# Optimization experiments

Measured on AMD Instinct MI355X. Metric: run time of the kernel, lower is better.

Reference implementation:

```python
import jax, jax.numpy as jnp
import numpy as np

NUM_CLASSES = 3
EPS = 1e-6
POS_IOU = 0.5   # assumed thresholds of utils.match_anchors_to_targets
NEG_IOU = 0.4
NEG_RATIO = 3


def _make_anchors(H, W, stride):
    sizes = np.array([3.0, 4.0, 5.0]) * stride  # 3 anchors per location
    ys = (np.arange(H) + 0.5) * stride
    xs = (np.arange(W) + 0.5) * stride
    cy, cx = np.meshgrid(ys, xs, indexing='ij')
    cx = cx[:, :, None]
    cy = cy[:, :, None]
    s = sizes[None, None, :]
    boxes = np.stack([cx - s / 2, cy - s / 2, cx + s / 2, cy + s / 2], axis=-1)  # [H,W,A,4]
    return boxes.reshape(-1, 4).astype(np.float32)


def setup_inputs() -> dict:
    key = jax.random.key(0)
    B, G, A, C = 64, 32, 3, NUM_CLASSES
    scales = [(128, 128, 8), (64, 64, 16), (32, 32, 32)]
    ks = jax.random.split(key, 6)
    inp = {}
    for i, (H, W, s) in enumerate(scales):
        inp[f'pred{i}'] = jax.random.normal(ks[i], (B, A * (5 + C), H, W), jnp.float32)
        inp[f'anchors{i}'] = jnp.asarray(_make_anchors(H, W, s))
    c = jax.random.uniform(ks[3], (B, G, 2), minval=100.0, maxval=900.0)
    wh = jax.random.uniform(ks[4], (B, G, 2), minval=16.0, maxval=200.0)
    inp['gt_boxes'] = jnp.concatenate([c - wh / 2, c + wh / 2], axis=-1)
    inp['gt_labels'] = jax.random.randint(ks[5], (B, G), 0, C)
    return inp


def _smooth_l1(x):
    ax = jnp.abs(x)
    return jnp.where(ax < 1.0, 0.5 * x * x, ax - 0.5)


def _bce_logits(x, t):
    return jnp.maximum(x, 0.0) - x * t + jnp.log1p(jnp.exp(-jnp.abs(x)))


def _pairwise_iou(a, b):  # a [N,4], b [G,4] -> [N,G]
    lt = jnp.maximum(a[:, None, :2], b[None, :, :2])
    rb = jnp.minimum(a[:, None, 2:], b[None, :, 2:])
    wh = jnp.clip(rb - lt, 0.0)
    inter = wh[..., 0] * wh[..., 1]
    area_a = (a[:, 2] - a[:, 0]) * (a[:, 3] - a[:, 1])
    area_b = (b[:, 2] - b[:, 0]) * (b[:, 3] - b[:, 1])
    return inter / (area_a[:, None] + area_b[None, :] - inter + 1e-9)


def _per_image(p, anc, gtb, gtl):
    # p: [N, 5+C], anc: [N,4], gtb: [G,4], gtl: [G]
    iou = _pairwise_iou(anc, gtb)
    best_iou = jnp.max(iou, axis=1)
    best_idx = jnp.argmax(iou, axis=1)
    m_boxes = gtb[best_idx]
    m_labels = gtl[best_idx]
    pos = best_iou >= POS_IOU
    neg = best_iou < NEG_IOU
    posf = pos.astype(p.dtype)

    ax = (anc[:, 0] + anc[:, 2]) * 0.5
    ay = (anc[:, 1] + anc[:, 3]) * 0.5
    aw = jnp.maximum(anc[:, 2] - anc[:, 0], EPS)
    ah = jnp.maximum(anc[:, 3] - anc[:, 1], EPS)
    gx = (m_boxes[:, 0] + m_boxes[:, 2]) * 0.5
    gy = (m_boxes[:, 1] + m_boxes[:, 3]) * 0.5
    gw = jnp.maximum(m_boxes[:, 2] - m_boxes[:, 0], EPS)
    gh = jnp.maximum(m_boxes[:, 3] - m_boxes[:, 1], EPS)
    t_tx = (gx - ax) / aw
    t_ty = (gy - ay) / ah
    t_tw = jnp.log(gw / aw)
    t_th = jnp.log(gh / ah)

    loc = (posf * (_smooth_l1(p[:, 0] - t_tx) + _smooth_l1(p[:, 1] - t_ty)
                   + _smooth_l1(p[:, 2] - t_tw) + _smooth_l1(p[:, 3] - t_th))).sum()

    obj_all = _bce_logits(p[:, 4], posf)
    # hard negative mining on detached loss: top (3*max(1,num_pos)) negatives
    num_pos = pos.sum()
    num_keep = NEG_RATIO * jnp.maximum(1, num_pos)
    neg_loss = jnp.where(neg, jax.lax.stop_gradient(obj_all), -1e9)
    order = jnp.argsort(-neg_loss)
    N = order.shape[0]
    ranks = jnp.zeros((N,), dtype=jnp.int32).at[order].set(jnp.arange(N, dtype=jnp.int32))
    selected = neg & (ranks < num_keep)
    obj = (obj_all * (posf + selected.astype(p.dtype))).sum()

    logp = jax.nn.log_softmax(p[:, 5:], axis=-1)
    tgt = jnp.maximum(m_labels, 0)
    ce = -jnp.take_along_axis(logp, tgt[:, None], axis=1)[:, 0]
    cls = (posf * ce).sum()
    return loc, obj, cls


def reference(pred0, pred1, pred2, anchors0, anchors1, anchors2, gt_boxes, gt_labels):
    B = pred0.shape[0]
    C = NUM_CLASSES
    total = jnp.float32(0.0)
    for pred, anc in ((pred0, anchors0), (pred1, anchors1), (pred2, anchors2)):
        N = anc.shape[0]
        p = pred.transpose(0, 2, 3, 1).reshape(B, N, 5 + C)  # [B, H*W*A, 5+C]
        loc, obj, cls = jax.vmap(lambda pb, gb, gl, a=anc: _per_image(pb, a, gb, gl))(
            p, gt_boxes, gt_labels)
        total = total + loc.sum() + obj.sum() + cls.sum()
    return total / jnp.maximum(1.0, float(B))
```

## Files before the change

### kernel.cpp

```cpp
#include <hip/hip_runtime.h>
#include <math.h>

#define BLK 256
#define SBLK 1024
#define NBINS 2048
#define SREP 8
#define SPAD 2049
#define CSH 42
#define QMASK ((1ULL << CSH) - 1ULL)

__device__ __forceinline__ float bce_logits(float x, float t){
    return fmaxf(x, 0.f) - x * t + log1pf(expf(-fabsf(x)));
}
__device__ __forceinline__ float smooth_l1(float x){
    float ax = fabsf(x);
    return ax < 1.f ? 0.5f * x * x : ax - 0.5f;
}

__global__ __launch_bounds__(BLK)
void det_map_all(const float* __restrict__ pred0,
                 const float* __restrict__ pred1,
                 const float* __restrict__ pred2,
                 const float* __restrict__ gtb,
                 const int*   __restrict__ gtl,
                 float* __restrict__ vals,
                 float* __restrict__ loss_slot,
                 int*   __restrict__ pcnt_slot,
                 unsigned* __restrict__ done_cnt,
                 int B)
{
    const int b  = blockIdx.y;
    const int bx = blockIdx.x;

    const float* pred; int s, qloc, P, logW; float stride_f; size_t vbase;
    if (bx < 48){      s=0; pred=pred0; P=16384; logW=7; stride_f= 8.f; qloc= bx      << 8; vbase=(size_t)b*49152; }
    else if (bx < 60){ s=1; pred=pred1; P= 4096; logW=6; stride_f=16.f; qloc=(bx-48) << 8; vbase=(size_t)B*49152 + (size_t)b*12288; }
    else {             s=2; pred=pred2; P= 1024; logW=5; stride_f=32.f; qloc=(bx-60) << 8; vbase=(size_t)B*49152 + (size_t)B*12288 + (size_t)b*3072; }

    const int tid = threadIdx.x;
    const int lq  = 2*logW - 2;
    const int Q4  = 1 << lq;
    const int a   = qloc >> lq;
    const int pix0 = (qloc - a*Q4 + tid) << 2;

    const float half = 0.5f * (float)(3 + a) * stride_f;

    const int pixLo = (qloc - a*Q4) << 2;
    const int y0 = pixLo >> logW, y1 = (pixLo + BLK*4 - 1) >> logW;
    const float ymin = ((float)y0 + 0.5f) * stride_f - half;
    const float ymax = ((float)y1 + 0.5f) * stride_f + half;

    __shared__ float4 sg[32];
    __shared__ float  sarea[32];
    __shared__ int    sl[32];
    __shared__ int    s_cnt;

    {
        bool keep = false; float4 G;
        if (tid < 32){
            G = ((const float4*)gtb)[b * 32 + tid];
            keep = (G.y < ymax) && (G.w > ymin);
        }
        unsigned long long m = __ballot(keep);
        if (tid < 64){
            if (keep){
                int idx = (int)__popcll(m & ((1ULL << tid) - 1ULL));
                sg[idx] = G;
                sarea[idx] = (G.z - G.x) * (G.w - G.y);
                sl[idx] = gtl[b * 32 + tid];
            }
            if (tid == 0) s_cnt = (int)__popcll(m);
        }
    }
    __syncthreads();
    const int cnt = s_cnt;

    const int x0 = pix0 & ((1 << logW) - 1);
    const int y  = pix0 >> logW;
    const float cy = ((float)y + 0.5f) * stride_f;
    const float Ay = cy - half, Ay2 = cy + half;
    const float area_a = (2.f * half) * (2.f * half);

    float ax[4], az[4];
    #pragma unroll
    for (int j = 0; j < 4; ++j){
        float cx = ((float)(x0 + j) + 0.5f) * stride_f;
        ax[j] = cx - half; az[j] = cx + half;
    }

    float bi[4] = {-1.f, -1.f, -1.f, -1.f};
    float bd[4] = { 1.f,  1.f,  1.f,  1.f};
    int   bg[4] = {0, 0, 0, 0};

    for (int g = 0; g < cnt; ++g){
        const float4 G = sg[g];
        const float sab = area_a + sarea[g];
        const float h = fmaxf(fminf(Ay2, G.w) - fmaxf(Ay, G.y), 0.f);
        #pragma unroll
        for (int j = 0; j < 4; ++j){
            float wdt = fmaxf(fminf(az[j], G.z) - fmaxf(ax[j], G.x), 0.f);
            float inter = wdt * h;
            float d = (sab - inter) + 1e-9f;
            if (inter * bd[j] > bi[j] * d){ bi[j] = inter; bd[j] = d; bg[j] = g; }
        }
    }

    const size_t cP = (size_t)P;
    const float* pp = pred + ((size_t)b * 24 + (size_t)a * 8) * cP + (size_t)pix0;
    const float4 p4v = *(const float4*)(pp + 4 * cP);
    const float p4a[4] = {p4v.x, p4v.y, p4v.z, p4v.w};

    float vout[4];
    float loss = 0.f; int pc = 0;
    #pragma unroll
    for (int j = 0; j < 4; ++j){
        const bool pos = 2.f * bi[j] >= bd[j];
        const bool neg = bi[j] < 0.4f * bd[j];
        vout[j] = neg ? bce_logits(p4a[j], 0.f) : -1.f;
        if (pos){
            pc++;
            const float4 G = sg[bg[j]];
            float axc = (ax[j] + az[j]) * 0.5f, ayc = (Ay + Ay2) * 0.5f;
            float aw = fmaxf(az[j] - ax[j], 1e-6f), ah = fmaxf(Ay2 - Ay, 1e-6f);
            float gxc = (G.x + G.z) * 0.5f, gyc = (G.y + G.w) * 0.5f;
            float gw = fmaxf(G.z - G.x, 1e-6f), gh = fmaxf(G.w - G.y, 1e-6f);
            float p0 = pp[0 * cP + j];
            float p1 = pp[1 * cP + j];
            float p2 = pp[2 * cP + j];
            float p3 = pp[3 * cP + j];
            loss += smooth_l1(p0 - (gxc - axc) / aw);
            loss += smooth_l1(p1 - (gyc - ayc) / ah);
            loss += smooth_l1(p2 - logf(gw / aw));
            loss += smooth_l1(p3 - logf(gh / ah));
            loss += bce_logits(p4a[j], 1.f);
            float c0 = pp[5 * cP + j];
            float c1 = pp[6 * cP + j];
            float c2 = pp[7 * cP + j];
            float m = fmaxf(c0, fmaxf(c1, c2));
            float lse = m + logf(expf(c0 - m) + expf(c1 - m) + expf(c2 - m));
            int tg = sl[bg[j]];
            float ct = (tg == 0) ? c0 : ((tg == 1) ? c1 : c2);
            loss += lse - ct;
        }
    }
    float4 vo = {vout[0], vout[1], vout[2], vout[3]};
    *(float4*)(vals + vbase + (size_t)(qloc - a*Q4 + tid) * 4 + (size_t)a * P) = vo;

    for (int off = 32; off > 0; off >>= 1){
        loss += __shfl_down(loss, off);
        pc   += __shfl_down(pc, off);
    }
    __shared__ float wsum[BLK / 64];
    __shared__ int   wcnt[BLK / 64];
    if ((tid & 63) == 0){ wsum[tid >> 6] = loss; wcnt[tid >> 6] = pc; }
    __syncthreads();
    if (tid == 0){
        float S = 0.f; int C = 0;
        for (int i = 0; i < BLK / 64; ++i){ S += wsum[i]; C += wcnt[i]; }
        loss_slot[b * 63 + bx] = S;
        pcnt_slot[b * 63 + bx] = C;
        if (b == 0 && bx == 0) *done_cnt = 0u;
    }
}

__global__ __launch_bounds__(SBLK)
void det_select(const float* __restrict__ vals,
                const float* __restrict__ loss_slot,
                const int* __restrict__ pcnt_slot,
                double* __restrict__ slice_tot,
                unsigned* __restrict__ done_cnt,
                float* __restrict__ out, int B)
{
    const int sb = blockIdx.x;
    const int s = sb / B, b = sb - s * B;
    const int N = (s == 0) ? 49152 : (s == 1) ? 12288 : 3072;
    size_t base = 0;
    if (s >= 1) base += (size_t)B * 49152;
    if (s >= 2) base += (size_t)B * 12288;
    const float* V = vals + base + (size_t)b * (size_t)N;

    const int tid = threadIdx.x;
    const int lane = tid & 63, w = tid >> 6;

    __shared__ unsigned long long h[SREP][SPAD];
    __shared__ unsigned long long waveT[16];
    __shared__ unsigned long long waveOff[17];
    __shared__ double sh_sel;
    __shared__ float sh_ml;
    __shared__ int sh_done, sh_K, sh_last;

    {
        const int nb   = (s == 0) ? 48 : (s == 1) ? 12 : 3;
        const int off0 = b * 63 + ((s == 0) ? 0 : (s == 1) ? 48 : 60);
        float ml = 0.f; int C = 0;
        if (tid < nb){ ml = loss_slot[off0 + tid]; C = pcnt_slot[off0 + tid]; }
        if (tid < 64){
            for (int off = 32; off > 0; off >>= 1){
                ml += __shfl_down(ml, off);
                C  += __shfl_down(C, off);
            }
            if (tid == 0){ sh_ml = ml; sh_K = 3 * max(1, C); sh_done = 0; }
        }
    }
    for (int i = tid; i < SREP * SPAD; i += SBLK)
        ((unsigned long long*)h)[i] = 0ULL;
    __syncthreads();

    const int rep = lane & (SREP - 1);
    for (int i = tid * 4; i < N; i += SBLK * 4){
        float4 v4 = *(const float4*)(V + i);
        #pragma unroll
        for (int j = 0; j < 4; ++j){
            float v = (j == 0) ? v4.x : (j == 1) ? v4.y : (j == 2) ? v4.z : v4.w;
            if (!(v >= 0.f)) continue;
            int bin = min((int)(v * 512.f), NBINS - 1);
            unsigned long long p = (1ULL << CSH) |
                (unsigned long long)(unsigned)(int)(v * 4194304.f);
            atomicAdd(&h[rep][bin], p);
        }
    }
    __syncthreads();

    const int bhi = NBINS - 1 - 2 * tid;
    unsigned long long c0p = 0ULL, c1p = 0ULL;
    #pragma unroll
    for (int r = 0; r < SREP; ++r){ c0p += h[r][bhi]; c1p += h[r][bhi - 1]; }
    const unsigned long long pair = c0p + c1p;
    unsigned long long ci = pair;
    #pragma unroll
    for (int off = 1; off < 64; off <<= 1){
        unsigned long long cu = __shfl_up(ci, off);
        if (lane >= off) ci += cu;
    }
    if (lane == 63) waveT[w] = ci;
    __syncthreads();
    if (tid == 0){
        unsigned long long acc = 0ULL;
        #pragma unroll
        for (int i = 0; i < 16; ++i){ waveOff[i] = acc; acc += waveT[i]; }
        waveOff[16] = acc;
        if (sh_K >= (int)(acc >> CSH)){
            sh_done = 1;
            sh_sel = (double)(acc & QMASK) * (1.0 / 4194304.0);
        }
    }
    __syncthreads();

    if (!sh_done){
        const int K = sh_K;
        const unsigned long long giP = waveOff[w] + ci;
        const unsigned long long geP = giP - pair;
        const int gi = (int)(giP >> CSH);
        const int ge = (int)(geP >> CSH);
        if (ge < K && K <= gi){
            const int c0 = (int)(c0p >> CSH);
            int bin, aboveC; unsigned long long aboveQ;
            if (ge + c0 >= K){ bin = bhi;     aboveC = ge;      aboveQ = geP & QMASK; }
            else             { bin = bhi - 1; aboveC = ge + c0; aboveQ = (geP + c0p) & QMASK; }
            float thresh = (float)bin * (1.f / 512.f);
            sh_sel = (double)aboveQ * (1.0 / 4194304.0)
                   + (double)(K - aboveC) * (double)thresh;
        }
        __syncthreads();
    }

    if (tid == 0){
        slice_tot[sb] = (double)sh_ml + sh_sel;
        __threadfence();
        unsigned t = atomicAdd(done_cnt, 1u);
        sh_last = (t == (unsigned)(gridDim.x - 1));
        if (sh_last) __threadfence();
    }
    __syncthreads();
    if (sh_last){
        double p = (tid < 3 * B) ? slice_tot[tid] : 0.0;
        for (int off = 32; off > 0; off >>= 1) p += __shfl_down(p, off);
        __shared__ double wred[16];
        if (lane == 0) wred[w] = p;
        __syncthreads();
        if (tid == 0){
            double tot = 0.0;
            for (int i = 0; i < 16; ++i) tot += wred[i];
            out[0] = (float)(tot / (double)B);
        }
    }
}

extern "C" void kernel_launch(void* const* d_in, const int* in_sizes, int n_in,
                              void* d_out, int out_size, void* d_ws, size_t ws_size,
                              hipStream_t stream)
{
    const float* gtb = (const float*)d_in[6];
    const int*   gtl = (const int*)d_in[7];
    const int B = in_sizes[6] / (32 * 4);

    unsigned* done      = (unsigned*)d_ws;
    double*   slice_tot = (double*)((char*)d_ws + 64);
    float*    loss_slot = (float*)((char*)d_ws + 2048);
    int*      pcnt_slot = (int*)((char*)d_ws + 2048 + 16384);
    float*    vals      = (float*)((char*)d_ws + 36864);

    det_map_all<<<dim3(63, B), BLK, 0, stream>>>(
        (const float*)d_in[0], (const float*)d_in[2], (const float*)d_in[4],
        gtb, gtl, vals, loss_slot, pcnt_slot, done, B);
    det_select<<<dim3(3 * B), SBLK, 0, stream>>>(
        vals, loss_slot, pcnt_slot, slice_tot, done, (float*)d_out, B);
}
```

Before: 202.9 us.

## Fuse negative-loss histogram building into map kernel, drop intermediate value buffer

Each map block now bins its negative-anchor BCE values into a shared-memory 64-bit histogram and merges it into a per-slice global histogram with atomics. This removes the per-anchor value buffer, so its global write in the map kernel and its reread plus re-histogramming in the select kernel both go away. The select kernel now reads the histogram directly. In exchange, every map block zeroes and flushes a 2048-bin histogram (32 KB of shared memory, which may lower occupancy), issues many global atomics, and the histogram needs a memset launch before the map kernel.

```diff
diff --git a/kernel.cpp b/kernel.cpp
--- a/kernel.cpp
+++ b/kernel.cpp
@@ -4,8 +4,7 @@
 #define BLK 256
 #define SBLK 1024
 #define NBINS 2048
-#define SREP 8
-#define SPAD 2049
+#define HREP 2
 #define CSH 42
 #define QMASK ((1ULL << CSH) - 1ULL)
 
@@ -23,7 +22,7 @@
                  const float* __restrict__ pred2,
                  const float* __restrict__ gtb,
                  const int*   __restrict__ gtl,
-                 float* __restrict__ vals,
+                 unsigned long long* __restrict__ hist,
                  float* __restrict__ loss_slot,
                  int*   __restrict__ pcnt_slot,
                  unsigned* __restrict__ done_cnt,
@@ -32,10 +31,10 @@
     const int b  = blockIdx.y;
     const int bx = blockIdx.x;
 
-    const float* pred; int s, qloc, P, logW; float stride_f; size_t vbase;
-    if (bx < 48){      s=0; pred=pred0; P=16384; logW=7; stride_f= 8.f; qloc= bx      << 8; vbase=(size_t)b*49152; }
-    else if (bx < 60){ s=1; pred=pred1; P= 4096; logW=6; stride_f=16.f; qloc=(bx-48) << 8; vbase=(size_t)B*49152 + (size_t)b*12288; }
-    else {             s=2; pred=pred2; P= 1024; logW=5; stride_f=32.f; qloc=(bx-60) << 8; vbase=(size_t)B*49152 + (size_t)B*12288 + (size_t)b*3072; }
+    const float* pred; int s, qloc, P, logW; float stride_f;
+    if (bx < 48){      s=0; pred=pred0; P=16384; logW=7; stride_f= 8.f; qloc= bx      << 8; }
+    else if (bx < 60){ s=1; pred=pred1; P= 4096; logW=6; stride_f=16.f; qloc=(bx-48) << 8; }
+    else {             s=2; pred=pred2; P= 1024; logW=5; stride_f=32.f; qloc=(bx-60) << 8; }
 
     const int tid = threadIdx.x;
     const int lq  = 2*logW - 2;
@@ -54,6 +53,10 @@
     __shared__ float  sarea[32];
     __shared__ int    sl[32];
     __shared__ int    s_cnt;
+    __shared__ unsigned long long sh_h[HREP][NBINS];
+
+    for (int i = tid; i < HREP * NBINS; i += BLK)
+        ((unsigned long long*)sh_h)[i] = 0ULL;
 
     {
         bool keep = false; float4 G;
@@ -110,13 +113,19 @@
     const float4 p4v = *(const float4*)(pp + 4 * cP);
     const float p4a[4] = {p4v.x, p4v.y, p4v.z, p4v.w};
 
-    float vout[4];
+    const int rep = tid & (HREP - 1);
     float loss = 0.f; int pc = 0;
     #pragma unroll
     for (int j = 0; j < 4; ++j){
         const bool pos = 2.f * bi[j] >= bd[j];
         const bool neg = bi[j] < 0.4f * bd[j];
-        vout[j] = neg ? bce_logits(p4a[j], 0.f) : -1.f;
+        if (neg){
+            float v = bce_logits(p4a[j], 0.f);
+            int bin = min((int)(v * 512.f), NBINS - 1);
+            unsigned long long pq = (1ULL << CSH) |
+                (unsigned long long)(unsigned)(int)(v * 4194304.f);
+            atomicAdd(&sh_h[rep][bin], pq);
+        }
         if (pos){
             pc++;
             const float4 G = sg[bg[j]];
@@ -143,8 +152,6 @@
             loss += lse - ct;
         }
     }
-    float4 vo = {vout[0], vout[1], vout[2], vout[3]};
-    *(float4*)(vals + vbase + (size_t)(qloc - a*Q4 + tid) * 4 + (size_t)a * P) = vo;
 
     for (int off = 32; off > 0; off >>= 1){
         loss += __shfl_down(loss, off);
@@ -154,6 +161,13 @@
     __shared__ int   wcnt[BLK / 64];
     if ((tid & 63) == 0){ wsum[tid >> 6] = loss; wcnt[tid >> 6] = pc; }
     __syncthreads();
+
+    unsigned long long* gh = hist + (size_t)(s * B + b) * NBINS;
+    for (int i = tid; i < NBINS; i += BLK){
+        unsigned long long t = sh_h[0][i] + sh_h[1][i];
+        if (t) atomicAdd(&gh[i], t);
+    }
+
     if (tid == 0){
         float S = 0.f; int C = 0;
         for (int i = 0; i < BLK / 64; ++i){ S += wsum[i]; C += wcnt[i]; }
@@ -164,7 +178,7 @@
 }
 
 __global__ __launch_bounds__(SBLK)
-void det_select(const float* __restrict__ vals,
+void det_select(const unsigned long long* __restrict__ hist,
                 const float* __restrict__ loss_slot,
                 const int* __restrict__ pcnt_slot,
                 double* __restrict__ slice_tot,
@@ -173,16 +187,10 @@
 {
     const int sb = blockIdx.x;
     const int s = sb / B, b = sb - s * B;
-    const int N = (s == 0) ? 49152 : (s == 1) ? 12288 : 3072;
-    size_t base = 0;
-    if (s >= 1) base += (size_t)B * 49152;
-    if (s >= 2) base += (size_t)B * 12288;
-    const float* V = vals + base + (size_t)b * (size_t)N;
 
     const int tid = threadIdx.x;
     const int lane = tid & 63, w = tid >> 6;
 
-    __shared__ unsigned long long h[SREP][SPAD];
     __shared__ unsigned long long waveT[16];
     __shared__ unsigned long long waveOff[17];
     __shared__ double sh_sel;
@@ -202,29 +210,10 @@
             if (tid == 0){ sh_ml = ml; sh_K = 3 * max(1, C); sh_done = 0; }
         }
     }
-    for (int i = tid; i < SREP * SPAD; i += SBLK)
-        ((unsigned long long*)h)[i] = 0ULL;
-    __syncthreads();
-
-    const int rep = lane & (SREP - 1);
-    for (int i = tid * 4; i < N; i += SBLK * 4){
-        float4 v4 = *(const float4*)(V + i);
-        #pragma unroll
-        for (int j = 0; j < 4; ++j){
-            float v = (j == 0) ? v4.x : (j == 1) ? v4.y : (j == 2) ? v4.z : v4.w;
-            if (!(v >= 0.f)) continue;
-            int bin = min((int)(v * 512.f), NBINS - 1);
-            unsigned long long p = (1ULL << CSH) |
-                (unsigned long long)(unsigned)(int)(v * 4194304.f);
-            atomicAdd(&h[rep][bin], p);
-        }
-    }
-    __syncthreads();
 
     const int bhi = NBINS - 1 - 2 * tid;
-    unsigned long long c0p = 0ULL, c1p = 0ULL;
-    #pragma unroll
-    for (int r = 0; r < SREP; ++r){ c0p += h[r][bhi]; c1p += h[r][bhi - 1]; }
+    const unsigned long long c0p = hist[(size_t)sb * NBINS + bhi];
+    const unsigned long long c1p = hist[(size_t)sb * NBINS + bhi - 1];
     const unsigned long long pair = c0p + c1p;
     unsigned long long ci = pair;
     #pragma unroll
@@ -298,11 +287,12 @@
     double*   slice_tot = (double*)((char*)d_ws + 64);
     float*    loss_slot = (float*)((char*)d_ws + 2048);
     int*      pcnt_slot = (int*)((char*)d_ws + 2048 + 16384);
-    float*    vals      = (float*)((char*)d_ws + 36864);
-
+    unsigned long long* hist = (unsigned long long*)((char*)d_ws + 36864);
+
+    hipMemsetAsync(hist, 0, (size_t)(3 * B) * NBINS * sizeof(unsigned long long), stream);
     det_map_all<<<dim3(63, B), BLK, 0, stream>>>(
         (const float*)d_in[0], (const float*)d_in[2], (const float*)d_in[4],
-        gtb, gtl, vals, loss_slot, pcnt_slot, done, B);
+        gtb, gtl, hist, loss_slot, pcnt_slot, done, B);
     det_select<<<dim3(3 * B), SBLK, 0, stream>>>(
-        vals, loss_slot, pcnt_slot, slice_tot, done, (float*)d_out, B);
-}
+        hist, loss_slot, pcnt_slot, slice_tot, done, (float*)d_out, B);
+}
```

After: 204.2 us (median of 2 runs). About the same (+0.6%).
